# Optimization experiments

Measured on AMD Instinct MI355X. Metric: run time of the kernel, lower is better.

## Reference

```python
import jax, jax.numpy as jnp
import numpy as np

# ---- model dims (match init_kwargs) ----
B, C, T = 64, 128, 512          # batch, n_channel, n_tokens
H = 256                          # n_hidden
GRID_SIZE = 5
SPLINE_ORDER = 3
N_COEFF = GRID_SIZE + SPLINE_ORDER   # 8 basis functions per input feature
GRID_RANGE = (-1.0, 1.0)
LN_EPS = 1e-5


def make_grid(in_features):
    # efficient-KAN extended knot grid: (in_features, grid_size + 2*order + 1)
    h = (GRID_RANGE[1] - GRID_RANGE[0]) / GRID_SIZE
    g = jnp.arange(-SPLINE_ORDER, GRID_SIZE + SPLINE_ORDER + 1, dtype=jnp.float32) * h + GRID_RANGE[0]
    return jnp.broadcast_to(g, (in_features, g.shape[0]))


def b_splines(x, grid):
    # x: (N, in), grid: (in, G+2k+1) -> (N, in, G+k) via Cox-de Boor recursion
    xg = x[:, :, None]
    bases = ((xg >= grid[:, :-1]) & (xg < grid[:, 1:])).astype(x.dtype)
    for k in range(1, SPLINE_ORDER + 1):
        left = (xg - grid[:, : -(k + 1)]) / (grid[:, k:-1] - grid[:, : -(k + 1)])
        right = (grid[:, k + 1:] - xg) / (grid[:, k + 1:] - grid[:, 1:-k])
        bases = left * bases[:, :, :-1] + right * bases[:, :, 1:]
    return bases


def kan_linear(x, grid, base_w, spline_w, spline_scaler):
    # x: (..., in) -> (..., out). base: silu(x)@W^T, plus spline combination.
    lead = x.shape[:-1]
    x2 = x.reshape(-1, x.shape[-1])
    base_out = jax.nn.silu(x2) @ base_w.T                              # (N, out)
    sw = spline_w * spline_scaler[:, :, None]                          # (out, in, coeff)
    spl_out = jnp.einsum('nic,oic->no', b_splines(x2, grid), sw)       # (N, out)
    return (base_out + spl_out).reshape(*lead, base_w.shape[0])


def setup_inputs() -> dict:
    key = jax.random.key(0)
    ks = jax.random.split(key, 8)
    scale1 = 1.0 / np.sqrt(C)
    scale2 = 1.0 / np.sqrt(H)
    return {
        "U": jax.random.normal(ks[0], (B, C, T), dtype=jnp.float32),
        "ln_w": jnp.ones((T, C), dtype=jnp.float32),
        "ln_b": jnp.zeros((T, C), dtype=jnp.float32),
        "bw1": jax.random.normal(ks[1], (H, C), dtype=jnp.float32) * scale1,
        "sw1": jax.random.normal(ks[2], (H, C, N_COEFF), dtype=jnp.float32) * (0.1 * scale1),
        "ss1": jnp.ones((H, C), dtype=jnp.float32),
        "bw2": jax.random.normal(ks[3], (C, H), dtype=jnp.float32) * scale2,
        "sw2": jax.random.normal(ks[4], (C, H, N_COEFF), dtype=jnp.float32) * (0.1 * scale2),
        "ss2": jnp.ones((C, H), dtype=jnp.float32),
    }


def reference(U, ln_w, ln_b, bw1, sw1, ss1, bw2, sw2, ss2):
    g1 = make_grid(C)
    g2 = make_grid(H)
    z = jnp.transpose(U, (0, 2, 1))                                   # (B, T, C)
    mu = jnp.mean(z, axis=(-2, -1), keepdims=True)
    var = jnp.var(z, axis=(-2, -1), keepdims=True)
    z = (z - mu) * jax.lax.rsqrt(var + LN_EPS) * ln_w + ln_b          # LN over [T, C]
    z = kan_linear(z, g1, bw1, sw1, ss1)                              # (B, T, H)
    z = kan_linear(z, g2, bw2, sw2, ss2)                              # (B, T, C)
    return U + jnp.transpose(z, (0, 2, 1))
```

## Files before the change

### kernel.cpp

```cpp
#include <hip/hip_runtime.h>
#include <math.h>

namespace {

constexpr int Bn = 64;
constexpr int Cn = 128;
constexpr int Tn = 512;
constexpr int Hn = 256;
constexpr int MR = 64;
constexpr int TB = Tn / MR;
constexpr int K1 = Cn * 9;
constexpr int K2 = Hn * 9;
constexpr int KSS = 296;
constexpr int HS = 258;
constexpr float LN_EPS = 1e-5f;

typedef __attribute__((ext_vector_type(8))) short short8;
typedef __attribute__((ext_vector_type(4))) float f32x4;

__device__ __forceinline__ unsigned short f2bf(float f) {
  unsigned int u = __builtin_bit_cast(unsigned int, f);
  u = (u + 0x7fffu + ((u >> 16) & 1u)) >> 16;
  return (unsigned short)u;
}

__device__ __forceinline__ void emit_act(float z, unsigned short* __restrict__ bufrow,
                                         int feat) {
  const float e = __expf(-z);
  const float sil = z * __builtin_amdgcn_rcpf(1.0f + e);
  bufrow[256 + feat] = f2bf(sil);
  const float p = z * 2.5f + 5.5f;
  const float fi = floorf(p);
  const int i = (int)fi;
  if (i >= 0 && i <= 10) {
    const float u = p - fi;
    const float u2 = u * u, u3 = u2 * u, t = 1.0f - u;
    const float w0 = t * t * t * (1.0f / 6.0f);
    const float w1 = (3.0f * u3 - 6.0f * u2 + 4.0f) * (1.0f / 6.0f);
    const float w2 = (-3.0f * u3 + 3.0f * u2 + 3.0f * u + 1.0f) * (1.0f / 6.0f);
    const float w3 = u3 * (1.0f / 6.0f);
    if (i >= 3) bufrow[(i - 3) * 32 + feat] = f2bf(w0);
    if (i >= 2 && i <= 9) bufrow[(i - 2) * 32 + feat] = f2bf(w1);
    if (i >= 1 && i <= 8) bufrow[(i - 1) * 32 + feat] = f2bf(w2);
    if (i <= 7) bufrow[i * 32 + feat] = f2bf(w3);
  }
}

}

__global__ __launch_bounds__(256) void kan_prep(
    const float* __restrict__ U, const float* __restrict__ bw1,
    const float* __restrict__ sw1, const float* __restrict__ ss1,
    const float* __restrict__ bw2, const float* __restrict__ sw2,
    const float* __restrict__ ss2, unsigned short* __restrict__ W1p,
    unsigned short* __restrict__ W2p, float* __restrict__ stats) {
  __shared__ float red[2][4];
  const int blk = blockIdx.x;
  if (blk < 256) {
    int idx = blk * 256 + threadIdx.x;
    if (idx < Hn * Cn) {
      const int h = idx >> 7, c = idx & 127;
      const float* sp = sw1 + ((size_t)h * Cn + c) * 8;
      const float sc = ss1[h * Cn + c];
      unsigned short* dst = W1p + (size_t)h * K1 + (c >> 5) * 288 + (c & 31);
#pragma unroll
      for (int j = 0; j < 8; ++j) dst[j * 32] = f2bf(sp[j] * sc);
      dst[8 * 32] = f2bf(bw1[h * Cn + c]);
    } else {
      idx -= Hn * Cn;
      const int c = idx >> 8, h = idx & 255;
      const float* sp = sw2 + ((size_t)c * Hn + h) * 8;
      const float sc = ss2[c * Hn + h];
      unsigned short* dst = W2p + (size_t)c * K2 + (h >> 5) * 288 + (h & 31);
#pragma unroll
      for (int j = 0; j < 8; ++j) dst[j * 32] = f2bf(sp[j] * sc);
      dst[8 * 32] = f2bf(bw2[c * Hn + h]);
    }
  } else {
    const int sblk = blk - 256;
    const int b = sblk >> 2, q = sblk & 3;
    const float4* p =
        (const float4*)(U + (size_t)b * (Cn * Tn) + q * (Cn * Tn / 4));
    float s = 0.f, s2 = 0.f;
#pragma unroll 4
    for (int i = threadIdx.x; i < (Cn * Tn / 4) / 4; i += 256) {
      const float4 v = p[i];
      s += v.x + v.y + v.z + v.w;
      s2 += v.x * v.x + v.y * v.y + v.z * v.z + v.w * v.w;
    }
#pragma unroll
    for (int off = 32; off > 0; off >>= 1) {
      s += __shfl_down(s, off);
      s2 += __shfl_down(s2, off);
    }
    if ((threadIdx.x & 63) == 0) {
      red[0][threadIdx.x >> 6] = s;
      red[1][threadIdx.x >> 6] = s2;
    }
    __syncthreads();
    if (threadIdx.x == 0) {
      stats[b * 8 + q * 2 + 0] = red[0][0] + red[0][1] + red[0][2] + red[0][3];
      stats[b * 8 + q * 2 + 1] = red[1][0] + red[1][1] + red[1][2] + red[1][3];
    }
  }
}

__global__ __launch_bounds__(1024, 4) void kan_fused(
    const float* __restrict__ U, const float* __restrict__ ln_w,
    const float* __restrict__ ln_b, const unsigned short* __restrict__ W1p,
    const unsigned short* __restrict__ W2p, const float* __restrict__ stats,
    float* __restrict__ out) {
  __shared__ unsigned short s_buf[2][MR * KSS];
  __shared__ float s_h1[MR * HS];

  const int tid = threadIdx.x;
  const int b = blockIdx.x / TB;
  const int t0 = (blockIdx.x % TB) * MR;

  const float* sp = stats + b * 8;
  const float ssum = sp[0] + sp[2] + sp[4] + sp[6];
  const float ssq = sp[1] + sp[3] + sp[5] + sp[7];
  const float inv_n = 1.0f / (float)(Cn * Tn);
  const float mean = ssum * inv_n;
  const float rstd = rsqrtf(ssq * inv_n - mean * mean + LN_EPS);

  const int w = tid >> 6;
  const int l = tid & 63;
  const int lo = l & 15;
  const int hi = l >> 4;
  const int feat = tid & 31;
  const int row0 = tid >> 5;

  const short8 zz = {0, 0, 0, 0, 0, 0, 0, 0};

  auto zero_rows = [&](unsigned short* nbuf) {
#pragma unroll
    for (int it = 0; it < 3; ++it) {
      const int i = l + it * 64;
      if (i < 148) {
        const int rr = i / 37;
        const int off = i - rr * 37;
        const int row = 2 * w + (rr & 1) + (rr >> 1) * 32;
        *(short8*)&nbuf[row * KSS + off * 8] = zz;
      }
    }
  };
  auto act1 = [&](int chunk, unsigned short* nbuf) {
    zero_rows(nbuf);
#pragma unroll
    for (int pp = 0; pp < 2; ++pp) {
      const int row = row0 + pp * 32;
      const int t = t0 + row;
      const int c = chunk * 32 + feat;
      const float uv = U[((size_t)b * Cn + c) * Tn + t];
      const float z = (uv - mean) * rstd * ln_w[t * Cn + c] + ln_b[t * Cn + c];
      emit_act(z, nbuf + row * KSS, feat);
    }
  };
  auto act2 = [&](int chunk, unsigned short* nbuf) {
    zero_rows(nbuf);
#pragma unroll
    for (int pp = 0; pp < 2; ++pp) {
      const int row = row0 + pp * 32;
      const float z = s_h1[row * HS + chunk * 32 + feat];
      emit_act(z, nbuf + row * KSS, feat);
    }
  };

  f32x4 acc1[4] = {};
  act1(0, s_buf[0]);
  __syncthreads();
  for (int k = 0; k < 4; ++k) {
    const unsigned short* cur = s_buf[k & 1];
    unsigned short* nxt = s_buf[(k + 1) & 1];
    const unsigned short* wb =
        W1p + (size_t)(w * 16 + lo) * K1 + k * 288 + hi * 8;
    short8 bnext = *(const short8*)wb;
    if (k < 3) act1(k + 1, nxt);
#pragma unroll
    for (int ks = 0; ks < 9; ++ks) {
      const short8 bcur = bnext;
      if (ks < 8) bnext = *(const short8*)(wb + (ks + 1) * 32);
      short8 a[4];
#pragma unroll
      for (int q = 0; q < 4; ++q)
        a[q] = *(const short8*)&cur[(q * 16 + lo) * KSS + ks * 32 + hi * 8];
#pragma unroll
      for (int q = 0; q < 4; ++q)
        acc1[q] =
            __builtin_amdgcn_mfma_f32_16x16x32_bf16(a[q], bcur, acc1[q], 0, 0, 0);
    }
    __syncthreads();
  }

#pragma unroll
  for (int q = 0; q < 4; ++q)
#pragma unroll
    for (int r = 0; r < 4; ++r)
      s_h1[(q * 16 + hi * 4 + r) * HS + w * 16 + lo] = acc1[q][r];
  __syncthreads();

  const int ng = w & 7;
  const int mh = w >> 3;
  f32x4 acc2[2] = {};
  act2(0, s_buf[0]);
  __syncthreads();
  for (int k = 0; k < 8; ++k) {
    const unsigned short* cur = s_buf[k & 1];
    unsigned short* nxt = s_buf[(k + 1) & 1];
    const unsigned short* wb =
        W2p + (size_t)(ng * 16 + lo) * K2 + k * 288 + hi * 8;
    short8 bnext = *(const short8*)wb;
    if (k < 7) act2(k + 1, nxt);
#pragma unroll
    for (int ks = 0; ks < 9; ++ks) {
      const short8 bcur = bnext;
      if (ks < 8) bnext = *(const short8*)(wb + (ks + 1) * 32);
      short8 a[2];
#pragma unroll
      for (int q = 0; q < 2; ++q)
        a[q] = *(const short8*)&cur[(mh * 32 + q * 16 + lo) * KSS + ks * 32 +
                                    hi * 8];
#pragma unroll
      for (int q = 0; q < 2; ++q)
        acc2[q] =
            __builtin_amdgcn_mfma_f32_16x16x32_bf16(a[q], bcur, acc2[q], 0, 0, 0);
    }
    __syncthreads();
  }

  const int c = ng * 16 + lo;
#pragma unroll
  for (int q = 0; q < 2; ++q) {
    const int trow = mh * 32 + q * 16 + hi * 4;
    const size_t base = ((size_t)b * Cn + c) * Tn + t0 + trow;
    const float4 uin = *(const float4*)(U + base);
    float4 o;
    o.x = uin.x + acc2[q][0];
    o.y = uin.y + acc2[q][1];
    o.z = uin.z + acc2[q][2];
    o.w = uin.w + acc2[q][3];
    *(float4*)(out + base) = o;
  }
}

extern "C" void kernel_launch(void* const* d_in, const int* in_sizes, int n_in,
                              void* d_out, int out_size, void* d_ws,
                              size_t ws_size, hipStream_t stream) {
  const float* U = (const float*)d_in[0];
  const float* ln_w = (const float*)d_in[1];
  const float* ln_b = (const float*)d_in[2];
  const float* bw1 = (const float*)d_in[3];
  const float* sw1 = (const float*)d_in[4];
  const float* ss1 = (const float*)d_in[5];
  const float* bw2 = (const float*)d_in[6];
  const float* sw2 = (const float*)d_in[7];
  const float* ss2 = (const float*)d_in[8];
  float* out = (float*)d_out;

  float* stats = (float*)d_ws;
  unsigned short* W1p = (unsigned short*)((char*)d_ws + 4096);
  unsigned short* W2p = W1p + (size_t)Hn * K1;

  kan_prep<<<512, 256, 0, stream>>>(U, bw1, sw1, ss1, bw2, sw2, ss2, W1p, W2p,
                                    stats);
  kan_fused<<<Bn * TB, 1024, 0, stream>>>(U, ln_w, ln_b, W1p, W2p, stats, out);
}
```

Baseline: 124.1 us.

## Use 128-row tiles with 32x32 MFMA, register-resident weights, bf16 hidden buffer

Doubles the row tile per block to 128 tokens and narrows each feature chunk to 16 features, so the activation buffer still fits in LDS. The 16x16x32 MFMA is replaced with 32x32x16, and each wave keeps a full chunk of B-operand weights in registers, prefetching the next chunk during compute. The intermediate hidden activations are stored in LDS as bf16 instead of fp32. This halves the grid size and raises weight reuse per block, at the cost of more register pressure, twice as many chunk iterations and barriers, and extra rounding of the hidden layer to bf16.

```diff
diff --git a/kernel.cpp b/kernel.cpp
--- a/kernel.cpp
+++ b/kernel.cpp
@@ -7,28 +7,37 @@
 constexpr int Cn = 128;
 constexpr int Tn = 512;
 constexpr int Hn = 256;
-constexpr int MR = 64;
+constexpr int MR = 128;
 constexpr int TB = Tn / MR;
 constexpr int K1 = Cn * 9;
 constexpr int K2 = Hn * 9;
-constexpr int KSS = 296;
-constexpr int HS = 258;
+constexpr int FC = 16;
+constexpr int KC = 144;
+constexpr int KSS = 152;
+constexpr int HS = 272;
+constexpr int NCH1 = 8;
+constexpr int NCH2 = 16;
 constexpr float LN_EPS = 1e-5f;
 
 typedef __attribute__((ext_vector_type(8))) short short8;
-typedef __attribute__((ext_vector_type(4))) float f32x4;
+typedef __attribute__((ext_vector_type(16))) float f32x16;
 
 __device__ __forceinline__ unsigned short f2bf(float f) {
   unsigned int u = __builtin_bit_cast(unsigned int, f);
   u = (u + 0x7fffu + ((u >> 16) & 1u)) >> 16;
   return (unsigned short)u;
 }
-
-__device__ __forceinline__ void emit_act(float z, unsigned short* __restrict__ bufrow,
+__device__ __forceinline__ float bf2f(unsigned short u) {
+  unsigned int v = (unsigned int)u << 16;
+  return __builtin_bit_cast(float, v);
+}
+
+__device__ __forceinline__ void emit_act(float z,
+                                         unsigned short* __restrict__ rowp,
                                          int feat) {
   const float e = __expf(-z);
   const float sil = z * __builtin_amdgcn_rcpf(1.0f + e);
-  bufrow[256 + feat] = f2bf(sil);
+  rowp[128 + feat] = f2bf(sil);
   const float p = z * 2.5f + 5.5f;
   const float fi = floorf(p);
   const int i = (int)fi;
@@ -37,12 +46,13 @@
     const float u2 = u * u, u3 = u2 * u, t = 1.0f - u;
     const float w0 = t * t * t * (1.0f / 6.0f);
     const float w1 = (3.0f * u3 - 6.0f * u2 + 4.0f) * (1.0f / 6.0f);
-    const float w2 = (-3.0f * u3 + 3.0f * u2 + 3.0f * u + 1.0f) * (1.0f / 6.0f);
+    const float w2 =
+        (-3.0f * u3 + 3.0f * u2 + 3.0f * u + 1.0f) * (1.0f / 6.0f);
     const float w3 = u3 * (1.0f / 6.0f);
-    if (i >= 3) bufrow[(i - 3) * 32 + feat] = f2bf(w0);
-    if (i >= 2 && i <= 9) bufrow[(i - 2) * 32 + feat] = f2bf(w1);
-    if (i >= 1 && i <= 8) bufrow[(i - 1) * 32 + feat] = f2bf(w2);
-    if (i <= 7) bufrow[i * 32 + feat] = f2bf(w3);
+    if (i >= 3) rowp[(i - 3) * 16 + feat] = f2bf(w0);
+    if (i >= 2 && i <= 9) rowp[(i - 2) * 16 + feat] = f2bf(w1);
+    if (i >= 1 && i <= 8) rowp[(i - 1) * 16 + feat] = f2bf(w2);
+    if (i <= 7) rowp[i * 16 + feat] = f2bf(w3);
   }
 }
 
@@ -60,21 +70,21 @@
     int idx = blk * 256 + threadIdx.x;
     if (idx < Hn * Cn) {
       const int h = idx >> 7, c = idx & 127;
-      const float* sp = sw1 + ((size_t)h * Cn + c) * 8;
+      const float* spw = sw1 + ((size_t)h * Cn + c) * 8;
       const float sc = ss1[h * Cn + c];
-      unsigned short* dst = W1p + (size_t)h * K1 + (c >> 5) * 288 + (c & 31);
-#pragma unroll
-      for (int j = 0; j < 8; ++j) dst[j * 32] = f2bf(sp[j] * sc);
-      dst[8 * 32] = f2bf(bw1[h * Cn + c]);
+      unsigned short* dst = W1p + (size_t)h * K1 + (c >> 4) * KC + (c & 15);
+#pragma unroll
+      for (int j = 0; j < 8; ++j) dst[j * 16] = f2bf(spw[j] * sc);
+      dst[8 * 16] = f2bf(bw1[h * Cn + c]);
     } else {
       idx -= Hn * Cn;
       const int c = idx >> 8, h = idx & 255;
-      const float* sp = sw2 + ((size_t)c * Hn + h) * 8;
+      const float* spw = sw2 + ((size_t)c * Hn + h) * 8;
       const float sc = ss2[c * Hn + h];
-      unsigned short* dst = W2p + (size_t)c * K2 + (h >> 5) * 288 + (h & 31);
-#pragma unroll
-      for (int j = 0; j < 8; ++j) dst[j * 32] = f2bf(sp[j] * sc);
-      dst[8 * 32] = f2bf(bw2[c * Hn + h]);
+      unsigned short* dst = W2p + (size_t)c * K2 + (h >> 4) * KC + (h & 15);
+#pragma unroll
+      for (int j = 0; j < 8; ++j) dst[j * 16] = f2bf(spw[j] * sc);
+      dst[8 * 16] = f2bf(bw2[c * Hn + h]);
     }
   } else {
     const int sblk = blk - 256;
@@ -111,11 +121,11 @@
     const unsigned short* __restrict__ W2p, const float* __restrict__ stats,
     float* __restrict__ out) {
   __shared__ unsigned short s_buf[2][MR * KSS];
-  __shared__ float s_h1[MR * HS];
+  __shared__ unsigned short s_h1[MR * HS];
 
   const int tid = threadIdx.x;
-  const int b = blockIdx.x / TB;
-  const int t0 = (blockIdx.x % TB) * MR;
+  const int b = blockIdx.x >> 2;
+  const int t0 = (blockIdx.x & 3) * MR;
 
   const float* sp = stats + b * 8;
   const float ssum = sp[0] + sp[2] + sp[4] + sp[6];
@@ -126,10 +136,10 @@
 
   const int w = tid >> 6;
   const int l = tid & 63;
-  const int lo = l & 15;
-  const int hi = l >> 4;
-  const int feat = tid & 31;
-  const int row0 = tid >> 5;
+  const int ln31 = l & 31;
+  const int hl = l >> 5;
+  const int feat = tid & 15;
+  const int rowq = tid >> 4;
 
   const short8 zz = {0, 0, 0, 0, 0, 0, 0, 0};
 
@@ -137,21 +147,21 @@
 #pragma unroll
     for (int it = 0; it < 3; ++it) {
       const int i = l + it * 64;
-      if (i < 148) {
-        const int rr = i / 37;
-        const int off = i - rr * 37;
-        const int row = 2 * w + (rr & 1) + (rr >> 1) * 32;
+      if (it < 2 || l < 16) {
+        const int r8 = i / 18;
+        const int off = i - r8 * 18;
+        const int row = w * 4 + (r8 & 3) + (r8 >> 2) * 64;
         *(short8*)&nbuf[row * KSS + off * 8] = zz;
       }
     }
   };
   auto act1 = [&](int chunk, unsigned short* nbuf) {
     zero_rows(nbuf);
+    const int c = chunk * FC + feat;
 #pragma unroll
     for (int pp = 0; pp < 2; ++pp) {
-      const int row = row0 + pp * 32;
+      const int row = rowq + pp * 64;
       const int t = t0 + row;
-      const int c = chunk * 32 + feat;
       const float uv = U[((size_t)b * Cn + c) * Tn + t];
       const float z = (uv - mean) * rstd * ln_w[t * Cn + c] + ln_b[t * Cn + c];
       emit_act(z, nbuf + row * KSS, feat);
@@ -161,85 +171,88 @@
     zero_rows(nbuf);
 #pragma unroll
     for (int pp = 0; pp < 2; ++pp) {
-      const int row = row0 + pp * 32;
-      const float z = s_h1[row * HS + chunk * 32 + feat];
+      const int row = rowq + pp * 64;
+      const float z = bf2f(s_h1[row * HS + chunk * FC + feat]);
       emit_act(z, nbuf + row * KSS, feat);
     }
   };
 
-  f32x4 acc1[4] = {};
+  const int mg = w >> 3;
+  const int ng = w & 7;
+  const unsigned short* wb1 = W1p + (size_t)(ng * 32 + ln31) * K1 + hl * 8;
+
+  short8 breg[9];
+#pragma unroll
+  for (int ks = 0; ks < 9; ++ks) breg[ks] = *(const short8*)(wb1 + ks * 16);
   act1(0, s_buf[0]);
   __syncthreads();
-  for (int k = 0; k < 4; ++k) {
+
+  f32x16 acc1[2] = {};
+  const int arow = mg * 64 + ln31;
+  for (int k = 0; k < NCH1; ++k) {
     const unsigned short* cur = s_buf[k & 1];
-    unsigned short* nxt = s_buf[(k + 1) & 1];
-    const unsigned short* wb =
-        W1p + (size_t)(w * 16 + lo) * K1 + k * 288 + hi * 8;
-    short8 bnext = *(const short8*)wb;
-    if (k < 3) act1(k + 1, nxt);
+    if (k < NCH1 - 1) act1(k + 1, s_buf[(k + 1) & 1]);
+    const unsigned short* a0p = cur + arow * KSS + hl * 8;
 #pragma unroll
     for (int ks = 0; ks < 9; ++ks) {
-      const short8 bcur = bnext;
-      if (ks < 8) bnext = *(const short8*)(wb + (ks + 1) * 32);
-      short8 a[4];
-#pragma unroll
-      for (int q = 0; q < 4; ++q)
-        a[q] = *(const short8*)&cur[(q * 16 + lo) * KSS + ks * 32 + hi * 8];
-#pragma unroll
-      for (int q = 0; q < 4; ++q)
-        acc1[q] =
-            __builtin_amdgcn_mfma_f32_16x16x32_bf16(a[q], bcur, acc1[q], 0, 0, 0);
+      const short8 a0 = *(const short8*)(a0p + ks * 16);
+      const short8 a1 = *(const short8*)(a0p + 32 * KSS + ks * 16);
+      const short8 bc = breg[ks];
+      if (k < NCH1 - 1)
+        breg[ks] = *(const short8*)(wb1 + (k + 1) * KC + ks * 16);
+      acc1[0] =
+          __builtin_amdgcn_mfma_f32_32x32x16_bf16(a0, bc, acc1[0], 0, 0, 0);
+      acc1[1] =
+          __builtin_amdgcn_mfma_f32_32x32x16_bf16(a1, bc, acc1[1], 0, 0, 0);
     }
     __syncthreads();
   }
 
-#pragma unroll
-  for (int q = 0; q < 4; ++q)
-#pragma unroll
-    for (int r = 0; r < 4; ++r)
-      s_h1[(q * 16 + hi * 4 + r) * HS + w * 16 + lo] = acc1[q][r];
+  const int mg2 = w >> 2;
+  const int ng2 = w & 3;
+  const unsigned short* wb2 = W2p + (size_t)(ng2 * 32 + ln31) * K2 + hl * 8;
+#pragma unroll
+  for (int ks = 0; ks < 9; ++ks) breg[ks] = *(const short8*)(wb2 + ks * 16);
+
+#pragma unroll
+  for (int q = 0; q < 2; ++q)
+#pragma unroll
+    for (int reg = 0; reg < 16; ++reg) {
+      const int row = mg * 64 + q * 32 + 4 * hl + (reg & 3) + 8 * (reg >> 2);
+      s_h1[row * HS + ng * 32 + ln31] = f2bf(acc1[q][reg]);
+    }
   __syncthreads();
-
-  const int ng = w & 7;
-  const int mh = w >> 3;
-  f32x4 acc2[2] = {};
   act2(0, s_buf[0]);
   __syncthreads();
-  for (int k = 0; k < 8; ++k) {
+
+  f32x16 acc2 = {};
+  const int arow2 = mg2 * 32 + ln31;
+  for (int k = 0; k < NCH2; ++k) {
     const unsigned short* cur = s_buf[k & 1];
-    unsigned short* nxt = s_buf[(k + 1) & 1];
-    const unsigned short* wb =
-        W2p + (size_t)(ng * 16 + lo) * K2 + k * 288 + hi * 8;
-    short8 bnext = *(const short8*)wb;
-    if (k < 7) act2(k + 1, nxt);
+    if (k < NCH2 - 1) act2(k + 1, s_buf[(k + 1) & 1]);
+    const unsigned short* ap = cur + arow2 * KSS + hl * 8;
 #pragma unroll
     for (int ks = 0; ks < 9; ++ks) {
-      const short8 bcur = bnext;
-      if (ks < 8) bnext = *(const short8*)(wb + (ks + 1) * 32);
-      short8 a[2];
-#pragma unroll
-      for (int q = 0; q < 2; ++q)
-        a[q] = *(const short8*)&cur[(mh * 32 + q * 16 + lo) * KSS + ks * 32 +
-                                    hi * 8];
-#pragma unroll
-      for (int q = 0; q < 2; ++q)
-        acc2[q] =
-            __builtin_amdgcn_mfma_f32_16x16x32_bf16(a[q], bcur, acc2[q], 0, 0, 0);
+      const short8 a = *(const short8*)(ap + ks * 16);
+      const short8 bc = breg[ks];
+      if (k < NCH2 - 1)
+        breg[ks] = *(const short8*)(wb2 + (k + 1) * KC + ks * 16);
+      acc2 = __builtin_amdgcn_mfma_f32_32x32x16_bf16(a, bc, acc2, 0, 0, 0);
     }
     __syncthreads();
   }
 
-  const int c = ng * 16 + lo;
-#pragma unroll
-  for (int q = 0; q < 2; ++q) {
-    const int trow = mh * 32 + q * 16 + hi * 4;
-    const size_t base = ((size_t)b * Cn + c) * Tn + t0 + trow;
+  const int c = ng2 * 32 + ln31;
+#pragma unroll
+  for (int g = 0; g < 4; ++g) {
+    const int tbase = t0 + mg2 * 32 + 4 * hl + 8 * g;
+    const size_t base = ((size_t)b * Cn + c) * Tn + tbase;
     const float4 uin = *(const float4*)(U + base);
     float4 o;
-    o.x = uin.x + acc2[q][0];
-    o.y = uin.y + acc2[q][1];
-    o.z = uin.z + acc2[q][2];
-    o.w = uin.w + acc2[q][3];
+    o.x = uin.x + acc2[g * 4 + 0];
+    o.y = uin.y + acc2[g * 4 + 1];
+    o.z = uin.z + acc2[g * 4 + 2];
+    o.w = uin.w + acc2[g * 4 + 3];
     *(float4*)(out + base) = o;
   }
 }
```

Result: no change. 124.6 us (+0.4%).
